# Optimization experiments

Measured on AMD Instinct MI355X. Metric: run time of the kernel, lower is better.

## Reference

```python
import jax, jax.numpy as jnp
import numpy as np

EPS = 1e-5
K = 32          # nsample in PCT sample_and_group
S1, S2 = 512, 256


def _bn_relu(h, gamma, beta, axes):
    # BatchNorm1d in training mode: batch stats over (batch, length) per channel (last axis here)
    mu = jnp.mean(h, axes, keepdims=True)
    var = jnp.var(h, axes, keepdims=True)
    return jax.nn.relu((h - mu) * jax.lax.rsqrt(var + EPS) * gamma + beta)


def _index_points(points, idx):
    # points [B,N,C], idx [B,...] int -> [B,...,C]
    return jax.vmap(lambda p, i: p[i])(points, idx)


def _fps(xyz, npoint):
    # farthest point sampling; deterministic start at index 0. xyz [B,N,3] -> [B,npoint] int32
    B, N, _ = xyz.shape

    def body(carry, _):
        dmin, far = carry
        c = jnp.take_along_axis(xyz, far[:, None, None], axis=1)  # [B,1,3]
        dmin = jnp.minimum(dmin, jnp.sum((xyz - c) ** 2, -1))     # [B,N]
        return (dmin, jnp.argmax(dmin, -1).astype(jnp.int32)), far

    init = (jnp.full((B, N), 1e10, xyz.dtype), jnp.zeros((B,), jnp.int32))
    _, idxs = jax.lax.scan(body, init, None, length=npoint)
    return jnp.transpose(idxs)  # [B, npoint]


def _sg(features, xyz, s, w1, g1, b1, w2, g2, b2):
    # features [B,N,C], xyz [B,N,3] -> (new_xyz [B,s,3], out [B,s,out_ch])
    xyz_c = jax.lax.stop_gradient(xyz)
    fps_idx = _fps(xyz_c, s)                       # [B,s]
    new_xyz = _index_points(xyz, fps_idx)          # [B,s,3]
    new_pts = _index_points(features, fps_idx)     # [B,s,C]
    q = jax.lax.stop_gradient(new_xyz)
    # squared distances centers->all points, [B,s,N]
    d = (jnp.sum(q * q, -1)[:, :, None] + jnp.sum(xyz_c * xyz_c, -1)[:, None, :]
         - 2.0 * jnp.einsum('bsc,bnc->bsn', q, xyz_c))
    _, knn = jax.lax.top_k(-d, K)                  # [B,s,K] nearest neighbors
    grouped = _index_points(features, knn)         # [B,s,K,C]
    rel = grouped - new_pts[:, :, None, :]
    feat = jnp.concatenate([rel, jnp.broadcast_to(new_pts[:, :, None, :], rel.shape)], -1)  # [B,s,K,2C]
    h = _bn_relu(jnp.einsum('bskc,oc->bsko', feat, w1), g1, b1, (0, 1, 2))
    h = _bn_relu(jnp.einsum('bskc,oc->bsko', h, w2), g2, b2, (0, 1, 2))
    return new_xyz, jnp.max(h, axis=2)             # max over K neighbors -> [B,s,out]


def _forward(x, w1, g1, b1, w2, g2, b2,
             s1_w1, s1_g1, s1_b1, s1_w2, s1_g2, s1_b2,
             s2_w1, s2_g1, s2_b1, s2_w2, s2_g2, s2_b2):
    xyz = jnp.transpose(x, (0, 2, 1))                                # [B,N,3]
    f = _bn_relu(jnp.einsum('bcn,oc->bno', x, w1), g1, b1, (0, 1))   # [B,N,64]
    f = _bn_relu(jnp.einsum('bnc,oc->bno', f, w2), g2, b2, (0, 1))   # [B,N,64]
    xyz1, f1 = _sg(f, xyz, S1, s1_w1, s1_g1, s1_b1, s1_w2, s1_g2, s1_b2)   # [B,512,128]
    _, f2 = _sg(f1, xyz1, S2, s2_w1, s2_g1, s2_b1, s2_w2, s2_g2, s2_b2)    # [B,256,256]
    return jnp.transpose(f2, (0, 2, 1))                              # [B,256,256] channel-first


def setup_inputs() -> dict:
    key = jax.random.key(0)
    ks = jax.random.split(key, 8)
    B, N = 32, 4096
    inp = {"x": jax.random.normal(ks[0], (B, 3, N), jnp.float32)}

    def w(k, o, i):
        return jax.random.normal(k, (o, i), jnp.float32) * (1.0 / np.sqrt(i))

    inp["w1"] = w(ks[1], 64, 3);   inp["g1"] = jnp.ones((64,), jnp.float32);  inp["b1"] = jnp.zeros((64,), jnp.float32)
    inp["w2"] = w(ks[2], 64, 64);  inp["g2"] = jnp.ones((64,), jnp.float32);  inp["b2"] = jnp.zeros((64,), jnp.float32)
    inp["s1_w1"] = w(ks[3], 128, 128); inp["s1_g1"] = jnp.ones((128,), jnp.float32); inp["s1_b1"] = jnp.zeros((128,), jnp.float32)
    inp["s1_w2"] = w(ks[4], 128, 128); inp["s1_g2"] = jnp.ones((128,), jnp.float32); inp["s1_b2"] = jnp.zeros((128,), jnp.float32)
    inp["s2_w1"] = w(ks[5], 256, 256); inp["s2_g1"] = jnp.ones((256,), jnp.float32); inp["s2_b1"] = jnp.zeros((256,), jnp.float32)
    inp["s2_w2"] = w(ks[6], 256, 256); inp["s2_g2"] = jnp.ones((256,), jnp.float32); inp["s2_b2"] = jnp.zeros((256,), jnp.float32)
    return inp


def reference(x, w1, g1, b1, w2, g2, b2,
              s1_w1, s1_g1, s1_b1, s1_w2, s1_g2, s1_b2,
              s2_w1, s2_g1, s2_b1, s2_w2, s2_g2, s2_b2):
    return _forward(x, w1, g1, b1, w2, g2, b2,
                    s1_w1, s1_g1, s1_b1, s1_w2, s1_g2, s1_b2,
                    s2_w1, s2_g1, s2_b1, s2_w2, s2_g2, s2_b2)
```

## Files before the change

kernel.cpp:

```cpp
#include <hip/hip_runtime.h>

typedef short short8 __attribute__((ext_vector_type(8)));
typedef _Float16 h8 __attribute__((ext_vector_type(8)));
typedef float f32x4 __attribute__((ext_vector_type(4)));

#define DEVI __device__ __forceinline__

DEVI float h2f(short s) { return (float)__builtin_bit_cast(_Float16, s); }
DEVI short f2h(float f) { return __builtin_bit_cast(short, (_Float16)f); }
DEVI f32x4 mfma16(short8 a, short8 b, f32x4 c) {
  return __builtin_amdgcn_mfma_f32_16x16x32_f16(
      __builtin_bit_cast(h8, a), __builtin_bit_cast(h8, b), c, 0, 0, 0);
}

DEVI float wave_max_bcast(float v) {
  const int ID = 0xff800000;
  int x = __builtin_bit_cast(int, v);
#define STEPM(ctrl)                                                     \
  {                                                                     \
    int t = __builtin_amdgcn_update_dpp(ID, x, ctrl, 0xf, 0xf, false);  \
    x = __builtin_bit_cast(int, fmaxf(__builtin_bit_cast(float, x),     \
                                      __builtin_bit_cast(float, t)));   \
  }
  STEPM(0x111) STEPM(0x112) STEPM(0x114) STEPM(0x118) STEPM(0x142) STEPM(0x143)
#undef STEPM
  return __builtin_bit_cast(float, __builtin_amdgcn_readlane(x, 63));
}
DEVI float wave_min_bcast_f(float v) {
  const int ID = 0x7f800000;
  int x = __builtin_bit_cast(int, v);
#define STEPN(ctrl)                                                     \
  {                                                                     \
    int t = __builtin_amdgcn_update_dpp(ID, x, ctrl, 0xf, 0xf, false);  \
    x = __builtin_bit_cast(int, fminf(__builtin_bit_cast(float, x),     \
                                      __builtin_bit_cast(float, t)));   \
  }
  STEPN(0x111) STEPN(0x112) STEPN(0x114) STEPN(0x118) STEPN(0x142) STEPN(0x143)
#undef STEPN
  return __builtin_bit_cast(float, __builtin_amdgcn_readlane(x, 63));
}
DEVI unsigned wave_min_bcast_u(unsigned v) {
  const int ID = (int)0xffffffff;
  int x = (int)v;
#define STEPU(ctrl)                                                     \
  {                                                                     \
    int t = __builtin_amdgcn_update_dpp(ID, x, ctrl, 0xf, 0xf, false);  \
    x = (int)((unsigned)x < (unsigned)t ? (unsigned)x : (unsigned)t);   \
  }
  STEPU(0x111) STEPU(0x112) STEPU(0x114) STEPU(0x118) STEPU(0x142) STEPU(0x143)
#undef STEPU
  return (unsigned)__builtin_amdgcn_readlane(x, 63);
}
DEVI unsigned wave_iscan_add(unsigned v) {
  int x = (int)v, t;
  t = __builtin_amdgcn_update_dpp(0, x, 0x111, 0xf, 0xf, false); x += t;
  t = __builtin_amdgcn_update_dpp(0, x, 0x112, 0xf, 0xf, false); x += t;
  t = __builtin_amdgcn_update_dpp(0, x, 0x114, 0xf, 0xf, false); x += t;
  t = __builtin_amdgcn_update_dpp(0, x, 0x118, 0xf, 0xf, false); x += t;
  t = __builtin_amdgcn_update_dpp(0, x, 0x142, 0xa, 0xf, false); x += t;
  t = __builtin_amdgcn_update_dpp(0, x, 0x143, 0xc, 0xf, false); x += t;
  return (unsigned)x;
}

__global__ __launch_bounds__(256) void prep_kernel(
    const float* __restrict__ w2, const float* __restrict__ s1w2,
    const float* __restrict__ s2w2, const float* __restrict__ s1w1,
    const float* __restrict__ s2w1, short* __restrict__ w2b,
    short* __restrict__ s1w2b, short* __restrict__ s2w2b,
    short* __restrict__ W1pp, short* __restrict__ W2pp) {
  int i = blockIdx.x * 256 + threadIdx.x;
  if (i < 4096) {
    w2b[i] = f2h(w2[i]);
  } else if (i < 20480) {
    int j = i - 4096; s1w2b[j] = f2h(s1w2[j]);
  } else if (i < 86016) {
    int j = i - 20480; s2w2b[j] = f2h(s2w2[j]);
  } else if (i < 102400) {
    int j = i - 86016; int c = j & 127;
    float v = s1w1[j]; if (c >= 64) v -= s1w1[j - 64];
    W1pp[j] = f2h(v);
  } else if (i < 167936) {
    int j = i - 102400; int c = j & 255;
    float v = s2w1[j]; if (c >= 128) v -= s2w1[j - 128];
    W2pp[j] = f2h(v);
  }
}

__global__ __launch_bounds__(256) void stageA_kernel(
    const float* __restrict__ x, const float* __restrict__ w1,
    float* __restrict__ xyz, short* __restrict__ h0) {
  int i = blockIdx.x * 256 + threadIdx.x;
  int b = i >> 12, n = i & 4095;
  const float* xb = x + ((size_t)b * 3 << 12) + n;
  float x0 = xb[0], x1 = xb[4096], x2 = xb[8192];
  float* xp = xyz + (size_t)i * 3;
  xp[0] = x0; xp[1] = x1; xp[2] = x2;
  short* hp = h0 + ((size_t)i << 6);
#pragma unroll
  for (int o8 = 0; o8 < 8; ++o8) {
    short8 t;
#pragma unroll
    for (int j = 0; j < 8; ++j) {
      int o = o8 * 8 + j;
      float h = x0 * w1[o * 3] + x1 * w1[o * 3 + 1] + x2 * w1[o * 3 + 2];
      t[j] = f2h(h);
    }
    *reinterpret_cast<short8*>(hp + o8 * 8) = t;
  }
}


DEVI void stats64_body(int bid, int nb, int tid, const short* __restrict__ h,
                       float* __restrict__ partials, int M) {
  __shared__ float l0[256], l1[256];
  const int c = tid & 63, g = tid >> 6;
  float s0 = 0.f, s1 = 0.f;
  for (int m = bid * 4 + g; m < M; m += nb * 4) {
    float v = h2f(h[(size_t)m * 64 + c]);
    s0 += v; s1 += v * v;
  }
  l0[tid] = s0; l1[tid] = s1;
  __syncthreads();
  if (g == 0) {
    for (int w = 1; w < 4; ++w) { s0 += l0[c + w * 64]; s1 += l1[c + w * 64]; }
    partials[(size_t)c * nb + bid] = s0;
    partials[(size_t)(64 + c) * nb + bid] = s1;
  }
}

DEVI void reduce2_body(int c, int tid, const float* __restrict__ partials,
                       const float* __restrict__ gamma, const float* __restrict__ beta,
                       float* __restrict__ scale, float* __restrict__ shift,
                       int NB, int C, float invM) {
  __shared__ float l0[4], l1[4];
  const float* p0 = partials + (size_t)c * NB;
  const float* p1 = partials + (size_t)(C + c) * NB;
  float s0 = 0.f, s1 = 0.f;
  for (int i = tid; i < NB; i += 256) { s0 += p0[i]; s1 += p1[i]; }
#pragma unroll
  for (int off = 1; off < 64; off <<= 1) {
    s0 += __shfl_xor(s0, off);
    s1 += __shfl_xor(s1, off);
  }
  if ((tid & 63) == 0) { l0[tid >> 6] = s0; l1[tid >> 6] = s1; }
  __syncthreads();
  if (tid == 0) {
    s0 = l0[0] + l0[1] + l0[2] + l0[3];
    s1 = l1[0] + l1[1] + l1[2] + l1[3];
    float mean = s0 * invM;
    float var = fmaxf(s1 * invM - mean * mean, 0.f);
    float sc = gamma[c] / sqrtf(var + 1e-5f);
    scale[c] = sc;
    shift[c] = beta[c] - mean * sc;
  }
}

__global__ __launch_bounds__(256) void reduce2_kernel(
    const float* __restrict__ partials, const float* __restrict__ gamma,
    const float* __restrict__ beta, float* __restrict__ scale,
    float* __restrict__ shift, int NB, int C, float invM) {
  reduce2_body(blockIdx.x, threadIdx.x, partials, gamma, beta, scale, shift, NB, C, invM);
}

DEVI void apply_body(int bid, int tid, const short* __restrict__ h,
                     short* __restrict__ f, const float* __restrict__ scale,
                     const float* __restrict__ shift) {
  size_t i = ((size_t)bid * 256 + tid) * 8;
  int c0 = (int)(i & 63);
  short8 v = *reinterpret_cast<const short8*>(h + i);
  short8 o;
#pragma unroll
  for (int j = 0; j < 8; ++j) {
    float y = h2f(v[j]) * scale[c0 + j] + shift[c0 + j];
    o[j] = f2h(fmaxf(y, 0.f));
  }
  *reinterpret_cast<short8*>(f + i) = o;
}

template <int NPTS, int T>
DEVI void fps_seg_body(char* smemraw, int bid, int tid, const float* __restrict__ xyz,
                       int* __restrict__ out, float* __restrict__ xyzc, int nsel,
                       int it0, int it1, float* __restrict__ dming,
                       int* __restrict__ farg) {
  __builtin_amdgcn_s_setprio(1);
  constexpr int PT = NPTS / T;
  constexpr int NW = T / 64;
  float* sx = (float*)smemraw;
  float* sy = sx + NPTS;
  float* sz = sy + NPTS;
  float* wv = sz + NPTS;
  unsigned* wi = (unsigned*)(wv + 2 * NW);
  const int lane = tid & 63, wave = tid >> 6;
  const float* base = xyz + (size_t)bid * NPTS * 3;
  float px[PT], py[PT], pz[PT], dmin[PT];
#pragma unroll
  for (int j = 0; j < PT; ++j) {
    int n = j * T + tid;
    px[j] = base[n * 3]; py[j] = base[n * 3 + 1]; pz[j] = base[n * 3 + 2];
    sx[n] = px[j]; sy[n] = py[j]; sz[n] = pz[j];
  }
  int far;
  if (it0 == 0) {
#pragma unroll
    for (int j = 0; j < PT; ++j) dmin[j] = 1e10f;
    far = 0;
  } else {
#pragma unroll
    for (int j = 0; j < PT; ++j) dmin[j] = dming[(size_t)bid * NPTS + j * T + tid];
    far = farg[bid];
  }
  __syncthreads();
  float cx = sx[far], cy = sy[far], cz = sz[far];
  for (int it = it0; it < it1; ++it) {
    if (tid == 0) {
      out[bid * nsel + it] = far;
      if (xyzc) {
        float* xc = xyzc + ((size_t)bid * nsel + it) * 3;
        xc[0] = cx; xc[1] = cy; xc[2] = cz;
      }
    }
    float bv = -1.f;
#pragma unroll
    for (int j = 0; j < PT; ++j) {
      float dx = __fsub_rn(px[j], cx), dy = __fsub_rn(py[j], cy), dz = __fsub_rn(pz[j], cz);
      float d = __fadd_rn(__fadd_rn(__fmul_rn(dx, dx), __fmul_rn(dy, dy)), __fmul_rn(dz, dz));
      float dm = fminf(dmin[j], d);
      dmin[j] = dm;
      bv = fmaxf(bv, dm);
    }
    float wmv = wave_max_bcast(bv);
    unsigned ci = 0xffffffffu;
#pragma unroll
    for (int j = PT - 1; j >= 0; --j)
      if (dmin[j] == wmv) ci = (unsigned)(j * T + tid);
    unsigned wmi = wave_min_bcast_u(ci);
    const int bsel = it & 1;
    if (lane == 0) { wv[bsel * NW + wave] = wmv; wi[bsel * NW + wave] = wmi; }
    __syncthreads();
    const int e = lane & (NW - 1);
    float v = wv[bsel * NW + e];
    unsigned si = wi[bsel * NW + e];
#define CMB(ctrl)                                                                        \
  {                                                                                      \
    float v2 = __builtin_bit_cast(                                                       \
        float, __builtin_amdgcn_update_dpp(0, __builtin_bit_cast(int, v), ctrl, 0xf, 0xf, true)); \
    unsigned i2 = (unsigned)__builtin_amdgcn_update_dpp(0, (int)si, ctrl, 0xf, 0xf, true);\
    bool bt = (v2 > v) || (v2 == v && i2 < si);                                          \
    v = bt ? v2 : v; si = bt ? i2 : si;                                                  \
  }
    if constexpr (NW >= 2) CMB(0x121)
    if constexpr (NW >= 4) CMB(0x122)
    if constexpr (NW >= 8) CMB(0x124)
#undef CMB
    far = (int)si;
    cx = sx[far]; cy = sy[far]; cz = sz[far];
  }
  if (it1 < nsel) {
#pragma unroll
    for (int j = 0; j < PT; ++j) dming[(size_t)bid * NPTS + j * T + tid] = dmin[j];
    if (tid == 0) farg[bid] = far;
  }
}

#define KNN_SMEM_BYTES ((4096 + 256 + 4 + 256 + 256) * 4)
template <int NPTS, int S>
DEVI void knn_body(char* smemraw, int bs, int tid, const float* __restrict__ pts,
                   const int* __restrict__ fpsidx, int* __restrict__ knn) {
  constexpr int PT = NPTS / 256;
  unsigned* hist = (unsigned*)smemraw;
  unsigned* csums = hist + 4096;
  unsigned* meta = csums + 256;
  float* bval = (float*)(meta + 4);
  unsigned* bidx = (unsigned*)(bval + 256);
  const int lane = tid & 63, wave = tid >> 6;
  const int b = bs / S;
  const int cidx = fpsidx[bs];
  const float* cp = pts + ((size_t)b * NPTS + cidx) * 3;
  const float qx = cp[0], qy = cp[1], qz = cp[2];
  const float qq = __fadd_rn(__fadd_rn(__fmul_rn(qx, qx), __fmul_rn(qy, qy)), __fmul_rn(qz, qz));
  const float* base = pts + (size_t)b * NPTS * 3;
  float d[PT]; unsigned u[PT];
#pragma unroll
  for (int j = 0; j < PT; ++j) {
    int n = j * 256 + tid;
    float x = base[n * 3], y = base[n * 3 + 1], z = base[n * 3 + 2];
    float pp = __fadd_rn(__fadd_rn(__fmul_rn(x, x), __fmul_rn(y, y)), __fmul_rn(z, z));
    float dot = __fadd_rn(__fadd_rn(__fmul_rn(qx, x), __fmul_rn(qy, y)), __fmul_rn(qz, z));
    d[j] = __fsub_rn(__fadd_rn(qq, pp), __fmul_rn(2.f, dot));
    unsigned bits = __builtin_bit_cast(unsigned, d[j]);
    unsigned m = (unsigned)((int)bits >> 31);
    u[j] = bits ^ (m | 0x80000000u);
  }
  {
    uint4 z4 = {0u, 0u, 0u, 0u};
    uint4* hq = (uint4*)hist;
    for (int i = tid; i < 1024; i += 256) hq[i] = z4;
    if (tid == 0) { meta[0] = 0; meta[3] = 0; }
  }
  __syncthreads();
#pragma unroll
  for (int j = 0; j < PT; ++j) atomicAdd(&hist[u[j] >> 20], 1u);
  __syncthreads();
  {
    const uint4* hq = (const uint4*)(hist + tid * 16);
    unsigned cs = 0;
#pragma unroll
    for (int q = 0; q < 4; ++q) {
      uint4 v = hq[q];
      cs += v.x + v.y + v.z + v.w;
    }
    csums[tid] = cs;
  }
  __syncthreads();
  if (wave == 0) {
    const int t4 = lane * 4;
    unsigned c0 = csums[t4], c1 = csums[t4 + 1], c2 = csums[t4 + 2], c3 = csums[t4 + 3];
    unsigned lt = c0 + c1 + c2 + c3;
    unsigned incl = wave_iscan_add(lt);
    unsigned excl = incl - lt;
    unsigned long long blt = __ballot(incl >= 32u);
    int L = __ffsll((long long)blt) - 1;
    if (lane == L) {
      unsigned cum = excl;
      int bucket = -1;
      unsigned cc[4] = {c0, c1, c2, c3};
#pragma unroll
      for (int q = 0; q < 4; ++q) {
        if (bucket < 0 && cum + cc[q] >= 32u) {
          int bbase = (t4 + q) * 16;
          for (int h = 0; h < 16; ++h) {
            unsigned hv = hist[bbase + h];
            if (cum + hv >= 32u) { bucket = bbase + h; break; }
            cum += hv;
          }
        } else if (bucket < 0) {
          cum += cc[q];
        }
      }
      meta[1] = (unsigned)bucket;
      meta[2] = cum;
    }
  }
  __syncthreads();
  const unsigned B = meta[1];
  const unsigned cb = meta[2];
  int* kout = knn + (size_t)bs * 32;
#pragma unroll
  for (int j = 0; j < PT; ++j) {
    unsigned bk = u[j] >> 20;
    if (bk < B) {
      unsigned p = atomicAdd(&meta[0], 1u);
      kout[p] = j * 256 + tid;
    } else if (bk == B) {
      unsigned p = atomicAdd(&meta[3], 1u);
      if (p < 256u) { bval[p] = d[j]; bidx[p] = (unsigned)(j * 256 + tid); }
    }
  }
  __syncthreads();
  const int m = 32 - (int)cb;
  if (wave == 0 && m > 0) {
    unsigned nb = meta[3]; if (nb > 256u) nb = 256u;
    float v0 = (lane < (int)nb) ? bval[lane] : 3.4e38f;
    unsigned i0 = (lane < (int)nb) ? bidx[lane] : 0xffffffffu;
    float v1 = (lane + 64 < (int)nb) ? bval[lane + 64] : 3.4e38f;
    unsigned i1 = (lane + 64 < (int)nb) ? bidx[lane + 64] : 0xffffffffu;
    float v2 = (lane + 128 < (int)nb) ? bval[lane + 128] : 3.4e38f;
    unsigned i2 = (lane + 128 < (int)nb) ? bidx[lane + 128] : 0xffffffffu;
    float v3 = (lane + 192 < (int)nb) ? bval[lane + 192] : 3.4e38f;
    unsigned i3 = (lane + 192 < (int)nb) ? bidx[lane + 192] : 0xffffffffu;
    for (int k = 0; k < m; ++k) {
      float lv = v0; unsigned li = i0;
      if (v1 < lv || (v1 == lv && i1 < li)) { lv = v1; li = i1; }
      if (v2 < lv || (v2 == lv && i2 < li)) { lv = v2; li = i2; }
      if (v3 < lv || (v3 == lv && i3 < li)) { lv = v3; li = i3; }
      float wmv = wave_min_bcast_f(lv);
      unsigned ci = (lv == wmv) ? li : 0xffffffffu;
      unsigned wmi = wave_min_bcast_u(ci);
      if (lane == 0) kout[cb + k] = (int)wmi;
      if (i0 == wmi) { v0 = 3.4e38f; i0 = 0xffffffffu; }
      if (i1 == wmi) { v1 = 3.4e38f; i1 = 0xffffffffu; }
      if (i2 == wmi) { v2 = 3.4e38f; i2 = 0xffffffffu; }
      if (i3 == wmi) { v3 = 3.4e38f; i3 = 0xffffffffu; }
    }
  }
}

template <int KD, int ND, bool GATHER, bool BNA, int NPTS, int S, int EPI>
DEVI void gemm_body(char* smemraw, int bid, int tid, int gemmBlocks,
                    const short* A, const int* KNNp, const int* FPSp,
                    const short* __restrict__ W, const float* __restrict__ bnscale,
                    const float* __restrict__ bnshift, short* Hout,
                    float* __restrict__ mmax, float* __restrict__ mmin,
                    float* __restrict__ partials) {
  constexpr int C = KD / 2;
  constexpr int NT = (ND > 128) ? 8 : ND / 16;
  constexpr int BR = (ND > 128) ? 64 : 128;
  constexpr int KC = (ND >= 256) ? 64 : KD;
  constexpr int LOG2KC = (KC == 64) ? 6 : 7;
  constexpr int NCH = KD / KC;
  constexpr int KTC = KC / 32;
  constexpr int LROW = KC + 8;
  constexpr int TROW = ND + 8;
  constexpr int LBB = ND * LROW * 2;
  constexpr int TBB = BR * TROW * 2;
  constexpr int LSOFF = (LBB > TBB) ? LBB : TBB;
  short* lb = (short*)smemraw;
  float* lstats = (float*)(smemraw + LSOFF);
  const int wave = tid >> 6, lane = tid & 63;
  const int rowOff = (ND > 128) ? (wave >> 1) * 32 : wave * 32;
  const int colOff = (ND > 128) ? (wave & 1) * 128 : 0;
  const int mBase = bid * BR + rowOff;
  for (int i = tid; i < 2 * ND; i += 256) lstats[i] = 0.f;

  const short* aptr[2][2];
#pragma unroll
  for (int rg = 0; rg < 2; ++rg) {
    int m = mBase + rg * 16 + (lane & 15);
    if constexpr (GATHER) {
      int idx = KNNp[m];
      int bb = m / (S * 32);
      int s = (m - bb * (S * 32)) >> 5;
      int fidx = FPSp[bb * S + s];
      aptr[rg][0] = A + ((size_t)bb * NPTS + idx) * C;
      aptr[rg][1] = A + ((size_t)bb * NPTS + fidx) * C;
    } else {
      aptr[rg][0] = A + (size_t)m * KD;
      aptr[rg][1] = A + (size_t)m * KD + C;
    }
  }
  const int koLane = (lane >> 4) * 8;
  f32x4 acc[2][NT];
#pragma unroll
  for (int rg = 0; rg < 2; ++rg)
#pragma unroll
    for (int nt = 0; nt < NT; ++nt) acc[rg][nt] = (f32x4){0.f, 0.f, 0.f, 0.f};

#pragma unroll
  for (int ch = 0; ch < NCH; ++ch) {
    __syncthreads();
    constexpr int SIT = (ND * KC) / 2048;
#pragma unroll
    for (int i = 0; i < SIT; ++i) {
      int e = i * 2048 + tid * 8;
      int n = e >> LOG2KC, kk = e & (KC - 1);
      short8 v = *reinterpret_cast<const short8*>(W + (size_t)n * KD + ch * KC + kk);
      *reinterpret_cast<short8*>(&lb[n * LROW + kk]) = v;
    }
    __syncthreads();
#pragma unroll
    for (int ktc = 0; ktc < KTC; ++ktc) {
      const int kt = ch * KTC + ktc;
      const int half = (kt * 32 >= C) ? 1 : 0;
      const int ko = kt * 32 + koLane;
      const int koh = ko - half * C;
      short8 afrag[2];
#pragma unroll
      for (int rg = 0; rg < 2; ++rg) {
        short8 a = *reinterpret_cast<const short8*>(aptr[rg][half] + koh);
        if constexpr (BNA) {
          const float* scp = bnscale + ko;
          const float* shp = bnshift + ko;
#pragma unroll
          for (int j = 0; j < 8; ++j) {
            float v = h2f(a[j]);
            v = fmaxf(v * scp[j] + shp[j], 0.f);
            a[j] = f2h(v);
          }
        }
        afrag[rg] = a;
      }
#pragma unroll
      for (int nt = 0; nt < NT; ++nt) {
        short8 bfr = *reinterpret_cast<const short8*>(
            &lb[(colOff + nt * 16 + (lane & 15)) * LROW + ktc * 32 + koLane]);
        acc[0][nt] = mfma16(afrag[0], bfr, acc[0][nt]);
        acc[1][nt] = mfma16(afrag[1], bfr, acc[1][nt]);
      }
    }
  }
  __syncthreads();

#pragma unroll
  for (int nt = 0; nt < NT; ++nt) {
    float s0 = 0.f, s1 = 0.f;
#pragma unroll
    for (int rg = 0; rg < 2; ++rg)
#pragma unroll
      for (int i = 0; i < 4; ++i) {
        float v = acc[rg][nt][i];
        s0 += v; s1 += v * v;
      }
    s0 += __shfl_xor(s0, 16); s0 += __shfl_xor(s0, 32);
    s1 += __shfl_xor(s1, 16); s1 += __shfl_xor(s1, 32);
    if (lane < 16) {
      atomicAdd(&lstats[colOff + nt * 16 + lane], s0);
      atomicAdd(&lstats[ND + colOff + nt * 16 + lane], s1);
    }
  }

  if constexpr (EPI == 0) {
#pragma unroll
    for (int rg = 0; rg < 2; ++rg)
#pragma unroll
      for (int nt = 0; nt < NT; ++nt)
#pragma unroll
        for (int i = 0; i < 4; ++i) {
          int r = rowOff + rg * 16 + (lane >> 4) * 4 + i;
          int n = colOff + nt * 16 + (lane & 15);
          lb[r * TROW + n] = f2h(acc[rg][nt][i]);
        }
    __syncthreads();
    constexpr int TPR = ND / 8;
    constexpr int RPI = 256 / TPR;
    const int r0 = tid / TPR, c0 = (tid % TPR) * 8;
#pragma unroll
    for (int it = 0; it < BR / RPI; ++it) {
      int r = it * RPI + r0;
      short8 v = *reinterpret_cast<const short8*>(&lb[r * TROW + c0]);
      *reinterpret_cast<short8*>(&Hout[(size_t)(bid * BR + r) * ND + c0]) = v;
    }
  } else {
    const int center = (bid * BR + rowOff) >> 5;
#pragma unroll
    for (int nt = 0; nt < NT; ++nt) {
      float mx = -3.4e38f, mn = 3.4e38f;
#pragma unroll
      for (int rg = 0; rg < 2; ++rg)
#pragma unroll
        for (int i = 0; i < 4; ++i) {
          float v = acc[rg][nt][i];
          mx = fmaxf(mx, v); mn = fminf(mn, v);
        }
      mx = fmaxf(mx, __shfl_xor(mx, 16)); mx = fmaxf(mx, __shfl_xor(mx, 32));
      mn = fminf(mn, __shfl_xor(mn, 16)); mn = fminf(mn, __shfl_xor(mn, 32));
      if (lane < 16) {
        mmax[(size_t)center * ND + colOff + nt * 16 + lane] = mx;
        mmin[(size_t)center * ND + colOff + nt * 16 + lane] = mn;
      }
    }
    __syncthreads();
  }
  for (int i = tid; i < 2 * ND; i += 256)
    partials[(size_t)i * gemmBlocks + bid] = lstats[i];
}


template <int FN, int FT>
__global__ __launch_bounds__(256, 1) void fps_stats_seg(
    int fpsBlocks, const float* fxyz, int* fout, float* fxyzc, int fnsel,
    int it0, int it1, float* dming, int* farg,
    const short* sh, float* sp, int sM, int snb) {
  extern __shared__ char smem[];
  if ((int)blockIdx.x < fpsBlocks)
    fps_seg_body<FN, FT>(smem, blockIdx.x, threadIdx.x, fxyz, fout, fxyzc, fnsel,
                         it0, it1, dming, farg);
  else
    stats64_body(blockIdx.x - fpsBlocks, snb, threadIdx.x, sh, sp, sM);
}

template <int FN, int FT>
__global__ __launch_bounds__(256, 1) void fps_r2_seg(
    int fpsBlocks, const float* fxyz, int* fout, float* fxyzc, int fnsel,
    int it0, int it1, float* dming, int* farg,
    const float* partials, const float* gamma, const float* beta,
    float* scale, float* shift, int NB, int C, float invM) {
  extern __shared__ char smem[];
  if ((int)blockIdx.x < fpsBlocks)
    fps_seg_body<FN, FT>(smem, blockIdx.x, threadIdx.x, fxyz, fout, fxyzc, fnsel,
                         it0, it1, dming, farg);
  else
    reduce2_body(blockIdx.x - fpsBlocks, threadIdx.x, partials, gamma, beta, scale,
                 shift, NB, C, invM);
}

template <int FN, int FT, int KD, int ND, bool BNA, int EPI>
__global__ __launch_bounds__(256, 1) void fps_gemm_seg(
    int fpsBlocks, const float* fxyz, int* fout, float* fxyzc, int fnsel,
    int it0, int it1, float* dming, int* farg,
    const short* A, const short* W, const float* bnscale, const float* bnshift,
    short* Hout, float* mmax, float* mmin, float* partials) {
  extern __shared__ char smem[];
  if ((int)blockIdx.x < fpsBlocks)
    fps_seg_body<FN, FT>(smem, blockIdx.x, threadIdx.x, fxyz, fout, fxyzc, fnsel,
                         it0, it1, dming, farg);
  else
    gemm_body<KD, ND, false, BNA, 1, 1, EPI>(smem, blockIdx.x - fpsBlocks, threadIdx.x,
                                             gridDim.x - fpsBlocks, A, nullptr, nullptr,
                                             W, bnscale, bnshift, Hout, mmax, mmin,
                                             partials);
}

template <int FN, int FT>
__global__ __launch_bounds__(256, 1) void fps_apply_seg(
    int fpsBlocks, const float* fxyz, int* fout, float* fxyzc, int fnsel,
    int it0, int it1, float* dming, int* farg,
    const short* ah, short* af, const float* ascale, const float* ashift) {
  extern __shared__ char smem[];
  if ((int)blockIdx.x < fpsBlocks)
    fps_seg_body<FN, FT>(smem, blockIdx.x, threadIdx.x, fxyz, fout, fxyzc, fnsel,
                         it0, it1, dming, farg);
  else
    apply_body(blockIdx.x - fpsBlocks, threadIdx.x, ah, af, ascale, ashift);
}

template <int KD, int ND, bool BNA, int EPI, int FN, int FT>
__global__ __launch_bounds__(256, 1) void gemm_fps_kernel(
    int fpsBlocks, const short* A, const short* W, const float* bnscale,
    const float* bnshift, short* Hout, float* mmax, float* mmin, float* partials,
    const float* fxyz, int* fout, float* fxyzc, int fnsel) {
  extern __shared__ char smem[];
  if ((int)blockIdx.x < fpsBlocks)
    fps_seg_body<FN, FT>(smem, blockIdx.x, threadIdx.x, fxyz, fout, fxyzc, fnsel,
                         0, fnsel, nullptr, nullptr);
  else
    gemm_body<KD, ND, false, BNA, 1, 1, EPI>(smem, blockIdx.x - fpsBlocks, threadIdx.x,
                                             gridDim.x - fpsBlocks, A, nullptr, nullptr,
                                             W, bnscale, bnshift, Hout, mmax, mmin,
                                             partials);
}

template <int KD, int ND, bool GATHER, bool BNA, int NPTS, int S, int EPI>
__global__ __launch_bounds__(256, 4) void gemm_kernel(
    const short* A, const int* KNNp, const int* FPSp, const short* W,
    const float* bnscale, const float* bnshift, short* Hout,
    float* mmax, float* mmin, float* partials) {
  extern __shared__ char smem[];
  int bid = (int)blockIdx.x;
  if constexpr (GATHER) {
    const int q = (int)gridDim.x >> 3;
    bid = (bid & 7) * q + (bid >> 3);
  }
  gemm_body<KD, ND, GATHER, BNA, NPTS, S, EPI>(smem, bid, threadIdx.x,
                                               gridDim.x, A, KNNp, FPSp, W, bnscale,
                                               bnshift, Hout, mmax, mmin, partials);
}

template <int NPTS, int S>
__global__ __launch_bounds__(256, 4) void knn_kernel2(
    const float* pts, const int* fpsidx, int* knn) {
  __shared__ __align__(16) char smem[KNN_SMEM_BYTES];
  knn_body<NPTS, S>(smem, blockIdx.x, threadIdx.x, pts, fpsidx, knn);
}

template <int NPTS, int S>
__global__ __launch_bounds__(256, 4) void maxpool_knn_kernel(
    int knnBlocks, const float* pts, const int* fpsidx, int* knn,
    const float* mmax, const float* mmin, const float* scale, const float* shift,
    short* f1) {
  __shared__ __align__(16) char smem[KNN_SMEM_BYTES];
  if ((int)blockIdx.x < knnBlocks) {
    knn_body<NPTS, S>(smem, blockIdx.x, threadIdx.x, pts, fpsidx, knn);
  } else {
    const int ctr = (blockIdx.x - knnBlocks) * 2 + (threadIdx.x >> 7);
    const int c = threadIdx.x & 127;
    const float sc = scale[c], sh = shift[c];
    float y = (sc >= 0.f) ? mmax[(size_t)ctr * 128 + c] : mmin[(size_t)ctr * 128 + c];
    f1[(size_t)ctr * 128 + c] = f2h(fmaxf(sc * y + sh, 0.f));
  }
}

__global__ __launch_bounds__(256) void maxpool_out_kernel(
    const float* __restrict__ mmax, const float* __restrict__ mmin,
    const float* __restrict__ scale, const float* __restrict__ shift,
    float* __restrict__ out) {
  const int bs = blockIdx.x, c = threadIdx.x;
  const int b = bs >> 8, s = bs & 255;
  const float sc = scale[c], sh = shift[c];
  float y = (sc >= 0.f) ? mmax[(size_t)bs * 256 + c] : mmin[(size_t)bs * 256 + c];
  out[((size_t)b << 16) + ((size_t)c << 8) + s] = fmaxf(sc * y + sh, 0.f);
}

extern "C" void kernel_launch(void* const* d_in, const int* in_sizes, int n_in,
                              void* d_out, int out_size, void* d_ws, size_t ws_size,
                              hipStream_t stream) {
  (void)in_sizes; (void)n_in; (void)out_size; (void)ws_size;
  const float* x    = (const float*)d_in[0];
  const float* w1   = (const float*)d_in[1];
  const float* g1   = (const float*)d_in[2];
  const float* b1   = (const float*)d_in[3];
  const float* w2   = (const float*)d_in[4];
  const float* g2   = (const float*)d_in[5];
  const float* b2   = (const float*)d_in[6];
  const float* s1w1 = (const float*)d_in[7];
  const float* s1g1 = (const float*)d_in[8];
  const float* s1b1 = (const float*)d_in[9];
  const float* s1w2 = (const float*)d_in[10];
  const float* s1g2 = (const float*)d_in[11];
  const float* s1b2 = (const float*)d_in[12];
  const float* s2w1 = (const float*)d_in[13];
  const float* s2g1 = (const float*)d_in[14];
  const float* s2b1 = (const float*)d_in[15];
  const float* s2w2 = (const float*)d_in[16];
  const float* s2g2 = (const float*)d_in[17];
  const float* s2b2 = (const float*)d_in[18];
  float* out = (float*)d_out;

  char* ws = (char*)d_ws;
  size_t off = 0;
  auto alloc = [&](size_t bytes) -> char* {
    size_t p = (off + 255) & ~(size_t)255;
    off = p + bytes;
    return ws + p;
  };

  float* xyz      = (float*)alloc(32ull * 4096 * 3 * 4);
  short* h0       = (short*)alloc(32ull * 4096 * 64 * 2);
  short* hb       = (short*)alloc(32ull * 4096 * 64 * 2);
  short* fb       = (short*)alloc(32ull * 4096 * 64 * 2);
  int*   fps1     = (int*)alloc(32ull * 512 * 4);
  float* xyzc1    = (float*)alloc(32ull * 512 * 3 * 4);
  int*   knn1     = (int*)alloc(32ull * 512 * 32 * 4);
  short* f1       = (short*)alloc(32ull * 512 * 128 * 2);
  int*   fps2     = (int*)alloc(32ull * 256 * 4);
  int*   knn2     = (int*)alloc(32ull * 256 * 32 * 4);
  float* dming    = (float*)alloc(32ull * 4096 * 4);
  int*   farg     = (int*)alloc(32 * 4);
  short* hbuf     = (short*)alloc(134217728ull);
  float* mm1max   = (float*)alloc(16384ull * 128 * 4);
  float* mm1min   = (float*)alloc(16384ull * 128 * 4);
  float* mm2max   = (float*)alloc(8192ull * 256 * 4);
  float* mm2min   = (float*)alloc(8192ull * 256 * 4);
  float* partials = (float*)alloc(2ull * 256 * 4096 * 4);
  float* scA  = (float*)alloc(64 * 4);  float* shA  = (float*)alloc(64 * 4);
  float* scBc = (float*)alloc(64 * 4);  float* shBc = (float*)alloc(64 * 4);
  float* sc1a = (float*)alloc(128 * 4); float* sh1a = (float*)alloc(128 * 4);
  float* sc1b = (float*)alloc(128 * 4); float* sh1b = (float*)alloc(128 * 4);
  float* sc2a = (float*)alloc(256 * 4); float* sh2a = (float*)alloc(256 * 4);
  float* sc2b = (float*)alloc(256 * 4); float* sh2b = (float*)alloc(256 * 4);
  short* w2b   = (short*)alloc(4096 * 2);
  short* s1w2b = (short*)alloc(16384 * 2);
  short* s2w2b = (short*)alloc(65536 * 2);
  short* W1pp  = (short*)alloc(16384 * 2);
  short* W2pp  = (short*)alloc(65536 * 2);

  prep_kernel<<<656, 256, 0, stream>>>(w2, s1w2, s2w2, s1w1, s2w1, w2b, s1w2b, s2w2b, W1pp, W2pp);
  stageA_kernel<<<512, 256, 0, stream>>>(x, w1, xyz, h0);

  fps_stats_seg<4096, 256><<<288, 256, 49216, stream>>>(
      32, xyz, fps1, xyzc1, 512, 0, 103, dming, farg, h0, partials, 131072, 256);
  fps_r2_seg<4096, 256><<<96, 256, 49216, stream>>>(
      32, xyz, fps1, xyzc1, 512, 103, 205, dming, farg,
      partials, g1, b1, scA, shA, 256, 64, 1.f / 131072.f);
  fps_gemm_seg<4096, 256, 64, 64, true, 0><<<1056, 256, 49216, stream>>>(
      32, xyz, fps1, xyzc1, 512, 205, 308, dming, farg,
      h0, w2b, scA, shA, hb, nullptr, nullptr, partials);
  fps_r2_seg<4096, 256><<<96, 256, 49216, stream>>>(
      32, xyz, fps1, xyzc1, 512, 308, 410, dming, farg,
      partials, g2, b2, scBc, shBc, 1024, 64, 1.f / 131072.f);
  fps_apply_seg<4096, 256><<<4128, 256, 49216, stream>>>(
      32, xyz, fps1, xyzc1, 512, 410, 512, dming, farg, hb, fb, scBc, shBc);

  knn_kernel2<4096, 512><<<16384, 256, 0, stream>>>(xyz, fps1, knn1);

  gemm_kernel<128, 128, true, false, 4096, 512, 0><<<4096, 256, 35840, stream>>>(
      fb, knn1, fps1, W1pp, nullptr, nullptr, hbuf, nullptr, nullptr, partials);
  reduce2_kernel<<<128, 256, 0, stream>>>(partials, s1g1, s1b1, sc1a, sh1a, 4096, 128, 1.f / 524288.f);

  gemm_fps_kernel<128, 128, true, 1, 512, 256><<<4128, 256, 35840, stream>>>(
      32, hbuf, s1w2b, sc1a, sh1a, nullptr, mm1max, mm1min, partials,
      xyzc1, fps2, nullptr, 256);
  reduce2_kernel<<<128, 256, 0, stream>>>(partials, s1g2, s1b2, sc1b, sh1b, 4096, 128, 1.f / 524288.f);

  maxpool_knn_kernel<512, 256><<<16384, 256, 0, stream>>>(
      8192, xyzc1, fps2, knn2, mm1max, mm1min, sc1b, sh1b, f1);

  gemm_kernel<256, 256, true, false, 512, 256, 0><<<4096, 256, 38912, stream>>>(
      f1, knn2, fps2, W2pp, nullptr, nullptr, hbuf, nullptr, nullptr, partials);
  reduce2_kernel<<<256, 256, 0, stream>>>(partials, s2g1, s2b1, sc2a, sh2a, 4096, 256, 1.f / 262144.f);
  gemm_kernel<256, 256, false, true, 1, 1, 1><<<4096, 256, 38912, stream>>>(
      hbuf, nullptr, nullptr, s2w2b, sc2a, sh2a, nullptr, mm2max, mm2min, partials);
  reduce2_kernel<<<256, 256, 0, stream>>>(partials, s2g2, s2b2, sc2b, sh2b, 4096, 256, 1.f / 262144.f);
  maxpool_out_kernel<<<8192, 256, 0, stream>>>(mm2max, mm2min, sc2b, sh2b, out);
}
```

Before: 877.9 us.

## Overlap stage-1 KNN with FPS segments and move second FPS into grouped GEMM

The first KNN pass is split into chunks of 128 centers and folded into the FPS segment kernels that run after those centers are chosen, so KNN work fills the idle CUs while the serial FPS continues. The second FPS is reimplemented as a single-wave register-resident loop and co-scheduled with the first gathered GEMM instead of the second GEMM. The FPS segment boundaries are rebalanced to even 128-iteration chunks. This removes a standalone KNN launch and hides serial FPS latency, at the cost of larger mixed-role grids, possible contention with the FPS blocks, and a single-wave FPS that may be slower per iteration.

```diff
diff --git a/kernel.cpp b/kernel.cpp
--- a/kernel.cpp
+++ b/kernel.cpp
@@ -259,6 +259,55 @@
 #pragma unroll
     for (int j = 0; j < PT; ++j) dming[(size_t)bid * NPTS + j * T + tid] = dmin[j];
     if (tid == 0) farg[bid] = far;
+  }
+}
+
+template <int NPTS>
+DEVI void fps2_wave_body(int bid, int lane, const float* __restrict__ xyz,
+                         int* __restrict__ out, int nsel) {
+  __builtin_amdgcn_s_setprio(1);
+  constexpr int PT = NPTS / 64;
+  const float* base = xyz + (size_t)bid * NPTS * 3;
+  float px[PT], py[PT], pz[PT], dmin[PT];
+#pragma unroll
+  for (int j = 0; j < PT; ++j) {
+    int n = j * 64 + lane;
+    px[j] = base[n * 3]; py[j] = base[n * 3 + 1]; pz[j] = base[n * 3 + 2];
+    dmin[j] = 1e10f;
+  }
+  int far = 0;
+  float cx = __builtin_bit_cast(float, __builtin_amdgcn_readlane(__builtin_bit_cast(int, px[0]), 0));
+  float cy = __builtin_bit_cast(float, __builtin_amdgcn_readlane(__builtin_bit_cast(int, py[0]), 0));
+  float cz = __builtin_bit_cast(float, __builtin_amdgcn_readlane(__builtin_bit_cast(int, pz[0]), 0));
+  for (int it = 0; it < nsel; ++it) {
+    if (lane == 0) out[bid * nsel + it] = far;
+    float bv = -1.f;
+#pragma unroll
+    for (int j = 0; j < PT; ++j) {
+      float dx = __fsub_rn(px[j], cx), dy = __fsub_rn(py[j], cy), dz = __fsub_rn(pz[j], cz);
+      float d = __fadd_rn(__fadd_rn(__fmul_rn(dx, dx), __fmul_rn(dy, dy)), __fmul_rn(dz, dz));
+      float dm = fminf(dmin[j], d);
+      dmin[j] = dm;
+      bv = fmaxf(bv, dm);
+    }
+    float wmv = wave_max_bcast(bv);
+    unsigned ci = 0xffffffffu;
+#pragma unroll
+    for (int j = PT - 1; j >= 0; --j)
+      if (dmin[j] == wmv) ci = (unsigned)(j * 64 + lane);
+    unsigned wmi = wave_min_bcast_u(ci);
+    far = (int)wmi;
+    const int jsel = (int)(wmi >> 6);
+    float xc = px[0], yc = py[0], zc = pz[0];
+#pragma unroll
+    for (int j = 1; j < PT; ++j) {
+      bool m = (jsel == j);
+      xc = m ? px[j] : xc; yc = m ? py[j] : yc; zc = m ? pz[j] : zc;
+    }
+    const int lsel = (int)(wmi & 63u);
+    cx = __builtin_bit_cast(float, __builtin_amdgcn_readlane(__builtin_bit_cast(int, xc), lsel));
+    cy = __builtin_bit_cast(float, __builtin_amdgcn_readlane(__builtin_bit_cast(int, yc), lsel));
+    cz = __builtin_bit_cast(float, __builtin_amdgcn_readlane(__builtin_bit_cast(int, zc), lsel));
   }
 }
 
@@ -558,65 +607,85 @@
     stats64_body(blockIdx.x - fpsBlocks, snb, threadIdx.x, sh, sp, sM);
 }
 
-template <int FN, int FT>
-__global__ __launch_bounds__(256, 1) void fps_r2_seg(
-    int fpsBlocks, const float* fxyz, int* fout, float* fxyzc, int fnsel,
-    int it0, int it1, float* dming, int* farg,
+template <int FN, int FT, int KNPTS, int KS>
+__global__ __launch_bounds__(256, 1) void fps_r2_knn_seg(
+    int fpsBlocks, int compBlocks, const float* fxyz, int* fout, float* fxyzc,
+    int fnsel, int it0, int it1, float* dming, int* farg,
     const float* partials, const float* gamma, const float* beta,
-    float* scale, float* shift, int NB, int C, float invM) {
+    float* scale, float* shift, int NB, int C, float invM,
+    const float* kpts, const int* kfps, int* kout, int ks0) {
   extern __shared__ char smem[];
-  if ((int)blockIdx.x < fpsBlocks)
-    fps_seg_body<FN, FT>(smem, blockIdx.x, threadIdx.x, fxyz, fout, fxyzc, fnsel,
+  const int bx = (int)blockIdx.x;
+  if (bx < fpsBlocks) {
+    fps_seg_body<FN, FT>(smem, bx, threadIdx.x, fxyz, fout, fxyzc, fnsel,
                          it0, it1, dming, farg);
-  else
-    reduce2_body(blockIdx.x - fpsBlocks, threadIdx.x, partials, gamma, beta, scale,
+  } else if (bx < fpsBlocks + compBlocks) {
+    reduce2_body(bx - fpsBlocks, threadIdx.x, partials, gamma, beta, scale,
                  shift, NB, C, invM);
-}
-
-template <int FN, int FT, int KD, int ND, bool BNA, int EPI>
-__global__ __launch_bounds__(256, 1) void fps_gemm_seg(
-    int fpsBlocks, const float* fxyz, int* fout, float* fxyzc, int fnsel,
-    int it0, int it1, float* dming, int* farg,
+  } else {
+    int kb = bx - fpsBlocks - compBlocks;
+    int bs = (kb >> 7) * KS + ks0 + (kb & 127);
+    knn_body<KNPTS, KS>(smem, bs, threadIdx.x, kpts, kfps, kout);
+  }
+}
+
+template <int FN, int FT, int KD, int ND, bool BNA, int EPI, int KNPTS, int KS>
+__global__ __launch_bounds__(256, 1) void fps_gemm_knn_seg(
+    int fpsBlocks, int compBlocks, const float* fxyz, int* fout, float* fxyzc,
+    int fnsel, int it0, int it1, float* dming, int* farg,
     const short* A, const short* W, const float* bnscale, const float* bnshift,
-    short* Hout, float* mmax, float* mmin, float* partials) {
+    short* Hout, float* partials,
+    const float* kpts, const int* kfps, int* kout, int ks0) {
   extern __shared__ char smem[];
-  if ((int)blockIdx.x < fpsBlocks)
-    fps_seg_body<FN, FT>(smem, blockIdx.x, threadIdx.x, fxyz, fout, fxyzc, fnsel,
+  const int bx = (int)blockIdx.x;
+  if (bx < fpsBlocks) {
+    fps_seg_body<FN, FT>(smem, bx, threadIdx.x, fxyz, fout, fxyzc, fnsel,
                          it0, it1, dming, farg);
-  else
-    gemm_body<KD, ND, false, BNA, 1, 1, EPI>(smem, blockIdx.x - fpsBlocks, threadIdx.x,
-                                             gridDim.x - fpsBlocks, A, nullptr, nullptr,
-                                             W, bnscale, bnshift, Hout, mmax, mmin,
-                                             partials);
-}
-
-template <int FN, int FT>
-__global__ __launch_bounds__(256, 1) void fps_apply_seg(
-    int fpsBlocks, const float* fxyz, int* fout, float* fxyzc, int fnsel,
-    int it0, int it1, float* dming, int* farg,
+  } else if (bx < fpsBlocks + compBlocks) {
+    gemm_body<KD, ND, false, BNA, 1, 1, EPI>(smem, bx - fpsBlocks, threadIdx.x,
+                                             compBlocks, A, nullptr, nullptr,
+                                             W, bnscale, bnshift, Hout, nullptr,
+                                             nullptr, partials);
+  } else {
+    int kb = bx - fpsBlocks - compBlocks;
+    int bs = (kb >> 7) * KS + ks0 + (kb & 127);
+    knn_body<KNPTS, KS>(smem, bs, threadIdx.x, kpts, kfps, kout);
+  }
+}
+
+template <int NPTS, int S>
+__global__ __launch_bounds__(256, 4) void apply_knn_kernel(
+    int knnBlocks, const float* kpts, const int* kfps, int* kout, int ks0,
     const short* ah, short* af, const float* ascale, const float* ashift) {
+  __shared__ __align__(16) char smem[KNN_SMEM_BYTES];
+  const int bx = (int)blockIdx.x;
+  if (bx < knnBlocks) {
+    int bs = (bx >> 7) * S + ks0 + (bx & 127);
+    knn_body<NPTS, S>(smem, bs, threadIdx.x, kpts, kfps, kout);
+  } else {
+    apply_body(bx - knnBlocks, threadIdx.x, ah, af, ascale, ashift);
+  }
+}
+
+template <int KD, int ND, int NPTS, int S>
+__global__ __launch_bounds__(256, 4) void mega1_kernel(
+    int fpsBlocks, const float* f2xyz, int* f2out, int f2nsel,
+    const short* A, const int* KNNp, const int* FPSp, const short* W,
+    short* Hout, float* partials) {
   extern __shared__ char smem[];
-  if ((int)blockIdx.x < fpsBlocks)
-    fps_seg_body<FN, FT>(smem, blockIdx.x, threadIdx.x, fxyz, fout, fxyzc, fnsel,
-                         it0, it1, dming, farg);
-  else
-    apply_body(blockIdx.x - fpsBlocks, threadIdx.x, ah, af, ascale, ashift);
-}
-
-template <int KD, int ND, bool BNA, int EPI, int FN, int FT>
-__global__ __launch_bounds__(256, 1) void gemm_fps_kernel(
-    int fpsBlocks, const short* A, const short* W, const float* bnscale,
-    const float* bnshift, short* Hout, float* mmax, float* mmin, float* partials,
-    const float* fxyz, int* fout, float* fxyzc, int fnsel) {
-  extern __shared__ char smem[];
-  if ((int)blockIdx.x < fpsBlocks)
-    fps_seg_body<FN, FT>(smem, blockIdx.x, threadIdx.x, fxyz, fout, fxyzc, fnsel,
-                         0, fnsel, nullptr, nullptr);
-  else
-    gemm_body<KD, ND, false, BNA, 1, 1, EPI>(smem, blockIdx.x - fpsBlocks, threadIdx.x,
-                                             gridDim.x - fpsBlocks, A, nullptr, nullptr,
-                                             W, bnscale, bnshift, Hout, mmax, mmin,
-                                             partials);
+  const int bx = (int)blockIdx.x;
+  if (bx < fpsBlocks) {
+    if (threadIdx.x < 64)
+      fps2_wave_body<512>(bx, threadIdx.x, f2xyz, f2out, f2nsel);
+  } else {
+    int gb = bx - fpsBlocks;
+    const int gB = (int)gridDim.x - fpsBlocks;
+    const int q = gB >> 3;
+    gb = (gb & 7) * q + (gb >> 3);
+    gemm_body<KD, ND, true, false, NPTS, S, 0>(smem, gb, threadIdx.x, gB, A, KNNp,
+                                               FPSp, W, nullptr, nullptr, Hout,
+                                               nullptr, nullptr, partials);
+  }
 }
 
 template <int KD, int ND, bool GATHER, bool BNA, int NPTS, int S, int EPI>
@@ -633,13 +702,6 @@
   gemm_body<KD, ND, GATHER, BNA, NPTS, S, EPI>(smem, bid, threadIdx.x,
                                                gridDim.x, A, KNNp, FPSp, W, bnscale,
                                                bnshift, Hout, mmax, mmin, partials);
-}
-
-template <int NPTS, int S>
-__global__ __launch_bounds__(256, 4) void knn_kernel2(
-    const float* pts, const int* fpsidx, int* knn) {
-  __shared__ __align__(16) char smem[KNN_SMEM_BYTES];
-  knn_body<NPTS, S>(smem, blockIdx.x, threadIdx.x, pts, fpsidx, knn);
 }
 
 template <int NPTS, int S>
@@ -737,28 +799,28 @@
   stageA_kernel<<<512, 256, 0, stream>>>(x, w1, xyz, h0);
 
   fps_stats_seg<4096, 256><<<288, 256, 49216, stream>>>(
-      32, xyz, fps1, xyzc1, 512, 0, 103, dming, farg, h0, partials, 131072, 256);
-  fps_r2_seg<4096, 256><<<96, 256, 49216, stream>>>(
-      32, xyz, fps1, xyzc1, 512, 103, 205, dming, farg,
-      partials, g1, b1, scA, shA, 256, 64, 1.f / 131072.f);
-  fps_gemm_seg<4096, 256, 64, 64, true, 0><<<1056, 256, 49216, stream>>>(
-      32, xyz, fps1, xyzc1, 512, 205, 308, dming, farg,
-      h0, w2b, scA, shA, hb, nullptr, nullptr, partials);
-  fps_r2_seg<4096, 256><<<96, 256, 49216, stream>>>(
-      32, xyz, fps1, xyzc1, 512, 308, 410, dming, farg,
-      partials, g2, b2, scBc, shBc, 1024, 64, 1.f / 131072.f);
-  fps_apply_seg<4096, 256><<<4128, 256, 49216, stream>>>(
-      32, xyz, fps1, xyzc1, 512, 410, 512, dming, farg, hb, fb, scBc, shBc);
-
-  knn_kernel2<4096, 512><<<16384, 256, 0, stream>>>(xyz, fps1, knn1);
-
-  gemm_kernel<128, 128, true, false, 4096, 512, 0><<<4096, 256, 35840, stream>>>(
-      fb, knn1, fps1, W1pp, nullptr, nullptr, hbuf, nullptr, nullptr, partials);
+      32, xyz, fps1, xyzc1, 512, 0, 128, dming, farg, h0, partials, 131072, 256);
+  fps_r2_knn_seg<4096, 256, 4096, 512><<<4192, 256, 49216, stream>>>(
+      32, 64, xyz, fps1, xyzc1, 512, 128, 256, dming, farg,
+      partials, g1, b1, scA, shA, 256, 64, 1.f / 131072.f,
+      xyz, fps1, knn1, 0);
+  fps_gemm_knn_seg<4096, 256, 64, 64, true, 0, 4096, 512><<<5152, 256, 49216, stream>>>(
+      32, 1024, xyz, fps1, xyzc1, 512, 256, 384, dming, farg,
+      h0, w2b, scA, shA, hb, partials,
+      xyz, fps1, knn1, 128);
+  fps_r2_knn_seg<4096, 256, 4096, 512><<<4192, 256, 49216, stream>>>(
+      32, 64, xyz, fps1, xyzc1, 512, 384, 512, dming, farg,
+      partials, g2, b2, scBc, shBc, 1024, 64, 1.f / 131072.f,
+      xyz, fps1, knn1, 256);
+  apply_knn_kernel<4096, 512><<<8192, 256, 0, stream>>>(
+      4096, xyz, fps1, knn1, 384, hb, fb, scBc, shBc);
+
+  mega1_kernel<128, 128, 4096, 512><<<4128, 256, 35840, stream>>>(
+      32, xyzc1, fps2, 256, fb, knn1, fps1, W1pp, hbuf, partials);
   reduce2_kernel<<<128, 256, 0, stream>>>(partials, s1g1, s1b1, sc1a, sh1a, 4096, 128, 1.f / 524288.f);
 
-  gemm_fps_kernel<128, 128, true, 1, 512, 256><<<4128, 256, 35840, stream>>>(
-      32, hbuf, s1w2b, sc1a, sh1a, nullptr, mm1max, mm1min, partials,
-      xyzc1, fps2, nullptr, 256);
+  gemm_kernel<128, 128, false, true, 1, 1, 1><<<4096, 256, 35840, stream>>>(
+      hbuf, nullptr, nullptr, s1w2b, sc1a, sh1a, nullptr, mm1max, mm1min, partials);
   reduce2_kernel<<<128, 256, 0, stream>>>(partials, s1g2, s1b2, sc1b, sh1b, 4096, 128, 1.f / 524288.f);
 
   maxpool_knn_kernel<512, 256><<<16384, 256, 0, stream>>>(
```

Result: faster. 838.4 us (-4.5%).
